# Kernel tuning notes

Hardware: AMD Instinct MI355X
Metric: run time of the kernel (lower is better)

Reference implementation:

```python
import jax, jax.numpy as jnp
import numpy as np

N_EMBD = 768
N_HEAD = 12


def setup_inputs() -> dict:
    key = jax.random.key(0)
    k1, k2, k3, k4, k5 = jax.random.split(key, 5)
    B, T, C = 2, 2048, N_EMBD
    s = 1.0 / np.sqrt(C)
    x = jax.random.normal(k1, (B, T, C), dtype=jnp.float32)
    W_attn = jax.random.uniform(k2, (C, 3 * C), dtype=jnp.float32, minval=-s, maxval=s)
    b_attn = jax.random.uniform(k3, (3 * C,), dtype=jnp.float32, minval=-s, maxval=s)
    W_proj = jax.random.uniform(k4, (C, C), dtype=jnp.float32, minval=-s, maxval=s)
    b_proj = jax.random.uniform(k5, (C,), dtype=jnp.float32, minval=-s, maxval=s)
    return {"x": x, "W_attn": W_attn, "b_attn": b_attn, "W_proj": W_proj, "b_proj": b_proj}


def reference(x, W_attn, b_attn, W_proj, b_proj):
    B, T, C = x.shape
    H = N_HEAD
    D = C // H
    qkv = x @ W_attn + b_attn                      # [B,T,3C]
    q, k, v = jnp.split(qkv, 3, axis=-1)
    q = q.reshape(B, T, H, D).transpose(0, 2, 1, 3)  # [B,H,T,D]
    k = k.reshape(B, T, H, D).transpose(0, 2, 1, 3)
    v = v.reshape(B, T, H, D).transpose(0, 2, 1, 3)
    scale = 1.0 / jnp.sqrt(jnp.asarray(D, dtype=x.dtype))
    scores = jnp.einsum("bhqd,bhkd->bhqk", q, k) * scale  # [B,H,T,T]
    causal = jnp.tril(jnp.ones((T, T), dtype=bool))
    scores = jnp.where(causal, scores, jnp.finfo(x.dtype).min)
    attn = jax.nn.softmax(scores, axis=-1)
    y = jnp.einsum("bhqk,bhkd->bhqd", attn, v)     # [B,H,T,D]
    y = y.transpose(0, 2, 1, 3).reshape(B, T, C)
    return y @ W_proj + b_proj
```

## Files before the change

### kernel.cpp

```cpp
#include <hip/hip_runtime.h>
#include <math.h>

#define N_EMBD 768
#define N_HEAD 12
#define HEAD_DIM 64
#define SEQ 2048
#define BATCH 2

typedef __attribute__((ext_vector_type(8))) short v8s;
typedef __attribute__((ext_vector_type(4))) float v4f;

__device__ __forceinline__ unsigned short f2bf(float f) {
    union { float f; unsigned int u; } x; x.f = f;
    unsigned int u = x.u + 0x7fffu + ((x.u >> 16) & 1u);
    return (unsigned short)(u >> 16);
}
__device__ __forceinline__ float bf2f(unsigned short s) {
    union { unsigned int u; float f; } x; x.u = ((unsigned int)s) << 16;
    return x.f;
}
__device__ __forceinline__ unsigned int pack_bf16(float lo, float hi) {
    unsigned int ul = __float_as_uint(lo) + 0x8000u;
    unsigned int uh = __float_as_uint(hi) + 0x8000u;
    return __builtin_amdgcn_perm(uh, ul, 0x07060302);
}

__device__ __forceinline__ void gload_lds16(const unsigned short* g, unsigned short* l) {
    __builtin_amdgcn_global_load_lds(
        (const __attribute__((address_space(1))) void*)g,
        (__attribute__((address_space(3))) void*)l, 16, 0, 0);
}

#define QSCALE 0.1803368801111396f

__global__ __launch_bounds__(256) void cast_x_kernel(
    const float* __restrict__ in, unsigned short* __restrict__ out)
{
    const int i = (blockIdx.x * 256 + threadIdx.x) * 8;
    const float4 a = *(const float4*)(in + i);
    const float4 b = *(const float4*)(in + i + 4);
    ushort4 s0, s1;
    s0.x = f2bf(a.x); s0.y = f2bf(a.y); s0.z = f2bf(a.z); s0.w = f2bf(a.w);
    s1.x = f2bf(b.x); s1.y = f2bf(b.y); s1.z = f2bf(b.z); s1.w = f2bf(b.w);
    *(ushort4*)(out + i) = s0;
    *(ushort4*)(out + i + 4) = s1;
}

__global__ __launch_bounds__(256) void transpose_cast_kernel(
    const float* __restrict__ in, unsigned short* __restrict__ out, int R, int C)
{
    __shared__ float t[32][33];
    const int bx = blockIdx.x * 32;
    const int by = blockIdx.y * 32;
    const int tx = threadIdx.x & 31, ty = threadIdx.x >> 5;
#pragma unroll
    for (int i = 0; i < 32; i += 8)
        t[ty + i][tx] = in[(size_t)(by + ty + i) * C + bx + tx];
    __syncthreads();
#pragma unroll
    for (int i = 0; i < 32; i += 8)
        out[(size_t)(bx + ty + i) * R + by + tx] = f2bf(t[tx][ty + i]);
}

__global__ __launch_bounds__(256) void qkv_gemm_mfma(
    const unsigned short* __restrict__ A,
    const unsigned short* __restrict__ Bt,
    const float* __restrict__ bias,
    unsigned short* __restrict__ qg,
    unsigned short* __restrict__ kg,
    unsigned short* __restrict__ vg)
{
    __shared__ unsigned short as[128 * 32];
    __shared__ unsigned short bs[128 * 32];
    const int K = 768;
    const int tid = threadIdx.x;
    const int lane = tid & 63;
    const int w = tid >> 6;
    const int wm = w >> 1, wn = w & 1;
    const int quad = lane >> 4, c = lane & 15;
    const int bm = blockIdx.y * 128;
    const int bn = blockIdx.x * 128;

    v4f acc[4][4];
#pragma unroll
    for (int i = 0; i < 4; i++)
#pragma unroll
        for (int j = 0; j < 4; j++) acc[i][j] = (v4f){0.f, 0.f, 0.f, 0.f};

    for (int k0 = 0; k0 < K; k0 += 32) {
        __syncthreads();
#pragma unroll
        for (int p = 0; p < 2; p++) {
            const int idx = p * 256 + tid;
            const int row = idx >> 2;
            const int off = (idx & 3) * 8;
            gload_lds16(A  + (size_t)(bm + row) * K + k0 + off, &as[idx * 8]);
            gload_lds16(Bt + (size_t)(bn + row) * K + k0 + off, &bs[idx * 8]);
        }
        __syncthreads();

        v8s af[4], bf[4];
#pragma unroll
        for (int fm = 0; fm < 4; fm++)
            af[fm] = *(const v8s*)&as[(wm * 64 + fm * 16 + c) * 32 + quad * 8];
#pragma unroll
        for (int fn = 0; fn < 4; fn++)
            bf[fn] = *(const v8s*)&bs[(wn * 64 + fn * 16 + c) * 32 + quad * 8];
#pragma unroll
        for (int fm = 0; fm < 4; fm++)
#pragma unroll
            for (int fn = 0; fn < 4; fn++)
                acc[fm][fn] = __builtin_amdgcn_mfma_f32_16x16x32_bf16(af[fm], bf[fn], acc[fm][fn], 0, 0, 0);
    }

    const int which = bn / N_EMBD;
    const int rem_base = bn - which * N_EMBD;
#pragma unroll
    for (int fm = 0; fm < 4; fm++) {
        const int m0 = bm + wm * 64 + fm * 16 + quad * 4;
        const int b = m0 >> 11;
        const int t0 = m0 & (SEQ - 1);
#pragma unroll
        for (int fn = 0; fn < 4; fn++) {
            const int rem = rem_base + wn * 64 + fn * 16 + c;
            const int h = rem >> 6, d = rem & 63;
            const float bv = bias[bn + wn * 64 + fn * 16 + c];
            const size_t bh = (size_t)(b * N_HEAD + h);
            if (which == 2) {
                ushort4 o;
                o.x = f2bf(acc[fm][fn][0] + bv);
                o.y = f2bf(acc[fm][fn][1] + bv);
                o.z = f2bf(acc[fm][fn][2] + bv);
                o.w = f2bf(acc[fm][fn][3] + bv);
                *(ushort4*)(vg + (bh * 64 + d) * SEQ + t0) = o;
            } else {
                unsigned short* dst = (which == 0) ? qg : kg;
                const float sc = (which == 0) ? QSCALE : 1.0f;
#pragma unroll
                for (int r = 0; r < 4; r++)
                    dst[(bh * SEQ + t0 + r) * 64 + d] = f2bf((acc[fm][fn][r] + bv) * sc);
            }
        }
    }
}

__global__ __launch_bounds__(256) void attn_kernel(
    const unsigned short* __restrict__ qg,
    const unsigned short* __restrict__ kg,
    const unsigned short* __restrict__ vg,
    unsigned short* __restrict__ pO,
    float* __restrict__ pl)
{
    __shared__ __align__(16) unsigned short ks[64 * 64];
    __shared__ __align__(16) unsigned short vs[64 * 64];
    __shared__ __align__(16) unsigned short ps[4][16 * 64];

    const int tid  = threadIdx.x;
    const int w    = tid >> 6;
    const int lane = tid & 63;
    const int quad = lane >> 4;
    const int c    = lane & 15;

    const int bid = (int)blockIdx.x;
    const int bh  = bid % 24;
    const int c2  = 79 - (bid / 24);
    int qt, kc;
    if (c2 < 8)       { qt = c2;                    kc = 0; }
    else if (c2 < 24) { qt = 8 + ((c2 - 8) >> 1);   kc = (c2 - 8) & 1; }
    else if (c2 < 48) { qt = 16 + (c2 - 24) / 3;    kc = (c2 - 24) % 3; }
    else              { qt = 24 + ((c2 - 48) >> 2); kc = (c2 - 48) & 3; }
    const int qbase = qt * 64;

    const unsigned short* qrow = qg + (size_t)bh * SEQ * 64;
    const unsigned short* krow = kg + (size_t)bh * SEQ * 64;
    const unsigned short* vrow = vg + (size_t)bh * 64 * SEQ;

    const unsigned short* qp = qrow + (size_t)(qbase + w * 16 + c) * 64 + quad * 8;
    const v8s bq0 = *(const v8s*)(qp);
    const v8s bq1 = *(const v8s*)(qp + 32);

    const int r0 = tid >> 3;
    const int ch0 = (tid & 7) ^ (r0 & 7);
    const unsigned short* kp0 = krow + (size_t)r0 * 64 + ch0 * 8;
    const unsigned short* vp0 = vrow + (size_t)r0 * SEQ + ch0 * 8;

    const int swz0 = ((quad ^ (c & 7)) * 8);
    const int swz1 = swz0 ^ 32;

    v4f oacc[4];
#pragma unroll
    for (int d = 0; d < 4; d++) oacc[d] = (v4f){0.f, 0.f, 0.f, 0.f};
    float l_acc = 0.f;

    const int q_lane = qbase + w * 16 + c;
    unsigned int* pw32 = (unsigned int*)&ps[w][0];
    const int psq = c & 7;

    const int kt0 = kc * 8;
    const int kt1 = min(kt0 + 8, qt + 1);
    for (int kt = kt0; kt < kt1; kt++) {
        const int key0 = kt * 64;
        __syncthreads();
        gload_lds16(kp0 + (size_t)key0 * 64, &ks[tid * 8]);
        gload_lds16(kp0 + (size_t)(key0 + 32) * 64, &ks[(256 + tid) * 8]);
        gload_lds16(vp0 + key0, &vs[tid * 8]);
        gload_lds16(vp0 + 32 * SEQ + key0, &vs[(256 + tid) * 8]);
        __syncthreads();

        v4f sacc[4];
#pragma unroll
        for (int n = 0; n < 4; n++) {
            const int rb = (n * 16 + c) * 64;
            const v8s ak0 = *(const v8s*)&ks[rb + swz0];
            const v8s ak1 = *(const v8s*)&ks[rb + swz1];
            v4f s = (v4f){0.f, 0.f, 0.f, 0.f};
            s = __builtin_amdgcn_mfma_f32_16x16x32_bf16(ak0, bq0, s, 0, 0, 0);
            s = __builtin_amdgcn_mfma_f32_16x16x32_bf16(ak1, bq1, s, 0, 0, 0);
            sacc[n] = s;
        }

        if (kt == qt) {
            const int kb = key0 + quad * 4;
#pragma unroll
            for (int n = 0; n < 4; n++)
#pragma unroll
                for (int r = 0; r < 4; r++)
                    if (kb + n * 16 + r > q_lane) sacc[n][r] = -1e30f;
        }

#pragma unroll
        for (int n = 0; n < 4; n++) {
            const float p0 = exp2f(sacc[n][0]);
            const float p1 = exp2f(sacc[n][1]);
            const float p2 = exp2f(sacc[n][2]);
            const float p3 = exp2f(sacc[n][3]);
            l_acc += (p0 + p1) + (p2 + p3);
            const int sswz = (2 * n + (quad >> 1)) ^ psq;
            const int dw = c * 32 + sswz * 4 + (quad & 1) * 2;
            pw32[dw]     = pack_bf16(p0, p1);
            pw32[dw + 1] = pack_bf16(p2, p3);
        }

        const v8s ap0 = *(const v8s*)&ps[w][c * 64 + swz0];
        const v8s ap1 = *(const v8s*)&ps[w][c * 64 + swz1];
#pragma unroll
        for (int d = 0; d < 4; d++) {
            const int rb = (d * 16 + c) * 64;
            const v8s bv0 = *(const v8s*)&vs[rb + swz0];
            const v8s bv1 = *(const v8s*)&vs[rb + swz1];
            oacc[d] = __builtin_amdgcn_mfma_f32_16x16x32_bf16(ap0, bv0, oacc[d], 0, 0, 0);
            oacc[d] = __builtin_amdgcn_mfma_f32_16x16x32_bf16(ap1, bv1, oacc[d], 0, 0, 0);
        }
    }

    l_acc += __shfl_xor(l_acc, 16, 64);
    l_acc += __shfl_xor(l_acc, 32, 64);

    const size_t pidx = (size_t)bh * 80 + c2;
    unsigned short* po = pO + pidx * 4096;
#pragma unroll
    for (int r = 0; r < 4; r++) {
        const int row = w * 16 + quad * 4 + r;
#pragma unroll
        for (int d = 0; d < 4; d++)
            po[row * 64 + d * 16 + c] = f2bf(oacc[d][r]);
    }
    if (lane < 16)
        pl[pidx * 64 + w * 16 + c] = l_acc;
}

__global__ __launch_bounds__(256) void combine_kernel(
    const unsigned short* __restrict__ pO,
    const float* __restrict__ pl,
    unsigned short* __restrict__ y)
{
    const int qt = (int)blockIdx.x;
    const int bh = (int)blockIdx.y;
    int base, nc;
    if (qt < 8)       { base = qt;                 nc = 1; }
    else if (qt < 16) { base = 8 + 2 * (qt - 8);   nc = 2; }
    else if (qt < 24) { base = 24 + 3 * (qt - 16); nc = 3; }
    else              { base = 48 + 4 * (qt - 24); nc = 4; }

    const int row = threadIdx.x >> 2;
    const int colg = (threadIdx.x & 3) * 16;

    float denom = 0.f;
    for (int i = 0; i < nc; i++)
        denom += pl[((size_t)bh * 80 + base + i) * 64 + row];
    const float inv = 1.0f / denom;

    float acc[16];
#pragma unroll
    for (int j = 0; j < 16; j++) acc[j] = 0.f;
    for (int i = 0; i < nc; i++) {
        const unsigned short* po = pO + ((size_t)bh * 80 + base + i) * 4096 + row * 64 + colg;
        ushort4 u0 = *(const ushort4*)(po + 0);
        ushort4 u1 = *(const ushort4*)(po + 4);
        ushort4 u2 = *(const ushort4*)(po + 8);
        ushort4 u3 = *(const ushort4*)(po + 12);
        acc[0]  += bf2f(u0.x); acc[1]  += bf2f(u0.y);
        acc[2]  += bf2f(u0.z); acc[3]  += bf2f(u0.w);
        acc[4]  += bf2f(u1.x); acc[5]  += bf2f(u1.y);
        acc[6]  += bf2f(u1.z); acc[7]  += bf2f(u1.w);
        acc[8]  += bf2f(u2.x); acc[9]  += bf2f(u2.y);
        acc[10] += bf2f(u2.z); acc[11] += bf2f(u2.w);
        acc[12] += bf2f(u3.x); acc[13] += bf2f(u3.y);
        acc[14] += bf2f(u3.z); acc[15] += bf2f(u3.w);
    }

    const int b = bh / N_HEAD;
    const int h = bh - b * N_HEAD;
    const int t = qt * 64 + row;
    unsigned short* yr = y + ((size_t)(b * SEQ + t)) * N_EMBD + h * 64 + colg;
    ushort4 o0, o1, o2, o3;
    o0.x = f2bf(acc[0] * inv);  o0.y = f2bf(acc[1] * inv);
    o0.z = f2bf(acc[2] * inv);  o0.w = f2bf(acc[3] * inv);
    o1.x = f2bf(acc[4] * inv);  o1.y = f2bf(acc[5] * inv);
    o1.z = f2bf(acc[6] * inv);  o1.w = f2bf(acc[7] * inv);
    o2.x = f2bf(acc[8] * inv);  o2.y = f2bf(acc[9] * inv);
    o2.z = f2bf(acc[10] * inv); o2.w = f2bf(acc[11] * inv);
    o3.x = f2bf(acc[12] * inv); o3.y = f2bf(acc[13] * inv);
    o3.z = f2bf(acc[14] * inv); o3.w = f2bf(acc[15] * inv);
    *(ushort4*)(yr + 0)  = o0;
    *(ushort4*)(yr + 4)  = o1;
    *(ushort4*)(yr + 8)  = o2;
    *(ushort4*)(yr + 12) = o3;
}

__global__ __launch_bounds__(256) void proj_gemm_mfma(
    const unsigned short* __restrict__ A,
    const unsigned short* __restrict__ Bt,
    const float* __restrict__ bias,
    float* __restrict__ out)
{
    __shared__ unsigned short as[128 * 32];
    __shared__ unsigned short bs[128 * 32];
    const int K = 768;
    const int tid = threadIdx.x;
    const int lane = tid & 63;
    const int w = tid >> 6;
    const int wm = w >> 1, wn = w & 1;
    const int quad = lane >> 4, c = lane & 15;
    const int bm = blockIdx.y * 128;
    const int bn = blockIdx.x * 128;

    v4f acc[4][4];
#pragma unroll
    for (int i = 0; i < 4; i++)
#pragma unroll
        for (int j = 0; j < 4; j++) acc[i][j] = (v4f){0.f, 0.f, 0.f, 0.f};

    for (int k0 = 0; k0 < K; k0 += 32) {
        __syncthreads();
#pragma unroll
        for (int p = 0; p < 2; p++) {
            const int idx = p * 256 + tid;
            const int row = idx >> 2;
            const int off = (idx & 3) * 8;
            gload_lds16(A  + (size_t)(bm + row) * K + k0 + off, &as[idx * 8]);
            gload_lds16(Bt + (size_t)(bn + row) * K + k0 + off, &bs[idx * 8]);
        }
        __syncthreads();

        v8s af[4], bf[4];
#pragma unroll
        for (int fm = 0; fm < 4; fm++)
            af[fm] = *(const v8s*)&as[(wm * 64 + fm * 16 + c) * 32 + quad * 8];
#pragma unroll
        for (int fn = 0; fn < 4; fn++)
            bf[fn] = *(const v8s*)&bs[(wn * 64 + fn * 16 + c) * 32 + quad * 8];
#pragma unroll
        for (int fm = 0; fm < 4; fm++)
#pragma unroll
            for (int fn = 0; fn < 4; fn++)
                acc[fm][fn] = __builtin_amdgcn_mfma_f32_16x16x32_bf16(af[fm], bf[fn], acc[fm][fn], 0, 0, 0);
    }

#pragma unroll
    for (int fm = 0; fm < 4; fm++) {
        const int m0 = bm + wm * 64 + fm * 16 + quad * 4;
#pragma unroll
        for (int fn = 0; fn < 4; fn++) {
            const int n = bn + wn * 64 + fn * 16 + c;
            const float bv = bias[n];
#pragma unroll
            for (int r = 0; r < 4; r++)
                out[(size_t)(m0 + r) * N_EMBD + n] = acc[fm][fn][r] + bv;
        }
    }
}

extern "C" void kernel_launch(void* const* d_in, const int* in_sizes, int n_in,
                              void* d_out, int out_size, void* d_ws, size_t ws_size,
                              hipStream_t stream) {
    const float* x      = (const float*)d_in[0];
    const float* W_attn = (const float*)d_in[1];
    const float* b_attn = (const float*)d_in[2];
    const float* W_proj = (const float*)d_in[3];
    const float* b_proj = (const float*)d_in[4];
    float* out = (float*)d_out;

    const size_t QSZ = (size_t)BATCH * N_HEAD * SEQ * HEAD_DIM;

    unsigned short* base = (unsigned short*)d_ws;
    unsigned short* xb  = base;
    unsigned short* wta = base + QSZ;
    unsigned short* pO  = base;
    float* pl = (float*)(base + (size_t)1920 * 4096);
    unsigned short* wtp = (unsigned short*)(pl + 1920 * 64);
    unsigned short* qg  = wtp + (size_t)N_EMBD * N_EMBD;
    unsigned short* kg  = qg + QSZ;
    unsigned short* vg  = kg + QSZ;
    unsigned short* yb  = vg + QSZ;

    cast_x_kernel<<<dim3((int)(QSZ / (256 * 8))), 256, 0, stream>>>(x, xb);
    transpose_cast_kernel<<<dim3(72, 24), 256, 0, stream>>>(W_attn, wta, N_EMBD, 3 * N_EMBD);
    transpose_cast_kernel<<<dim3(24, 24), 256, 0, stream>>>(W_proj, wtp, N_EMBD, N_EMBD);

    qkv_gemm_mfma<<<dim3(18, 32), 256, 0, stream>>>(xb, wta, b_attn, qg, kg, vg);
    attn_kernel<<<dim3(80 * 24), 256, 0, stream>>>(qg, kg, vg, pO, pl);
    combine_kernel<<<dim3(32, BATCH * N_HEAD), 256, 0, stream>>>(pO, pl, yb);
    proj_gemm_mfma<<<dim3(6, 32), 256, 0, stream>>>(yb, wtp, b_proj, out);
}
```

Measured before the change: 176.5 us.

## Double-buffer LDS tiles in GEMMs and attention, merge prep kernels

The QKV and projection GEMMs and the attention kernel now keep two LDS buffers. Each loop iteration issues the next tile's global-to-LDS loads right after the barrier, so the copy overlaps with the MFMA work on the current tile, and one barrier per iteration is removed. Separately, the x cast and the two weight transpose-cast kernels are merged into one prep kernel launch that picks its task by block index, which saves two launches. The cost is double the LDS per block, which can lower occupancy. Correctness also relies on the barrier waiting for the outstanding async LDS loads.

```diff
diff --git a/kernel.cpp b/kernel.cpp
--- a/kernel.cpp
+++ b/kernel.cpp
@@ -33,25 +33,37 @@
 
 #define QSCALE 0.1803368801111396f
 
-__global__ __launch_bounds__(256) void cast_x_kernel(
-    const float* __restrict__ in, unsigned short* __restrict__ out)
-{
-    const int i = (blockIdx.x * 256 + threadIdx.x) * 8;
-    const float4 a = *(const float4*)(in + i);
-    const float4 b = *(const float4*)(in + i + 4);
-    ushort4 s0, s1;
-    s0.x = f2bf(a.x); s0.y = f2bf(a.y); s0.z = f2bf(a.z); s0.w = f2bf(a.w);
-    s1.x = f2bf(b.x); s1.y = f2bf(b.y); s1.z = f2bf(b.z); s1.w = f2bf(b.w);
-    *(ushort4*)(out + i) = s0;
-    *(ushort4*)(out + i + 4) = s1;
-}
-
-__global__ __launch_bounds__(256) void transpose_cast_kernel(
-    const float* __restrict__ in, unsigned short* __restrict__ out, int R, int C)
+__global__ __launch_bounds__(256) void prep_kernel(
+    const float* __restrict__ x,
+    const float* __restrict__ W_attn,
+    const float* __restrict__ W_proj,
+    unsigned short* __restrict__ xb,
+    unsigned short* __restrict__ wta,
+    unsigned short* __restrict__ wtp)
 {
     __shared__ float t[32][33];
-    const int bx = blockIdx.x * 32;
-    const int by = blockIdx.y * 32;
+    const int blk = (int)blockIdx.x;
+    if (blk < 1536) {
+        const int i = (blk * 256 + threadIdx.x) * 8;
+        const float4 a = *(const float4*)(x + i);
+        const float4 b = *(const float4*)(x + i + 4);
+        ushort4 s0, s1;
+        s0.x = f2bf(a.x); s0.y = f2bf(a.y); s0.z = f2bf(a.z); s0.w = f2bf(a.w);
+        s1.x = f2bf(b.x); s1.y = f2bf(b.y); s1.z = f2bf(b.z); s1.w = f2bf(b.w);
+        *(ushort4*)(xb + i) = s0;
+        *(ushort4*)(xb + i + 4) = s1;
+        return;
+    }
+    const float* in; unsigned short* out; int R, C, bx, by;
+    if (blk < 1536 + 1728) {
+        const int b2 = blk - 1536;
+        in = W_attn; out = wta; R = 768; C = 2304;
+        bx = (b2 % 72) * 32; by = (b2 / 72) * 32;
+    } else {
+        const int b2 = blk - 3264;
+        in = W_proj; out = wtp; R = 768; C = 768;
+        bx = (b2 % 24) * 32; by = (b2 / 24) * 32;
+    }
     const int tx = threadIdx.x & 31, ty = threadIdx.x >> 5;
 #pragma unroll
     for (int i = 0; i < 32; i += 8)
@@ -70,8 +82,8 @@
     unsigned short* __restrict__ kg,
     unsigned short* __restrict__ vg)
 {
-    __shared__ unsigned short as[128 * 32];
-    __shared__ unsigned short bs[128 * 32];
+    __shared__ unsigned short as[2][128 * 32];
+    __shared__ unsigned short bs[2][128 * 32];
     const int K = 768;
     const int tid = threadIdx.x;
     const int lane = tid & 63;
@@ -81,31 +93,42 @@
     const int bm = blockIdx.y * 128;
     const int bn = blockIdx.x * 128;
 
+    const int srow = tid >> 2;
+    const int soff = (tid & 3) * 8;
+    const unsigned short* ap = A  + (size_t)(bm + srow) * K + soff;
+    const unsigned short* bp = Bt + (size_t)(bn + srow) * K + soff;
+    const unsigned short* ap2 = A  + (size_t)(bm + 64 + srow) * K + soff;
+    const unsigned short* bp2 = Bt + (size_t)(bn + 64 + srow) * K + soff;
+
     v4f acc[4][4];
 #pragma unroll
     for (int i = 0; i < 4; i++)
 #pragma unroll
         for (int j = 0; j < 4; j++) acc[i][j] = (v4f){0.f, 0.f, 0.f, 0.f};
 
-    for (int k0 = 0; k0 < K; k0 += 32) {
+    gload_lds16(ap, &as[0][tid * 8]);
+    gload_lds16(ap2, &as[0][(256 + tid) * 8]);
+    gload_lds16(bp, &bs[0][tid * 8]);
+    gload_lds16(bp2, &bs[0][(256 + tid) * 8]);
+
+    int bufi = 0;
+    for (int k0 = 0; k0 < K; k0 += 32, bufi ^= 1) {
         __syncthreads();
-#pragma unroll
-        for (int p = 0; p < 2; p++) {
-            const int idx = p * 256 + tid;
-            const int row = idx >> 2;
-            const int off = (idx & 3) * 8;
-            gload_lds16(A  + (size_t)(bm + row) * K + k0 + off, &as[idx * 8]);
-            gload_lds16(Bt + (size_t)(bn + row) * K + k0 + off, &bs[idx * 8]);
-        }
-        __syncthreads();
+        if (k0 + 32 < K) {
+            const int kn = k0 + 32;
+            gload_lds16(ap + kn, &as[bufi ^ 1][tid * 8]);
+            gload_lds16(ap2 + kn, &as[bufi ^ 1][(256 + tid) * 8]);
+            gload_lds16(bp + kn, &bs[bufi ^ 1][tid * 8]);
+            gload_lds16(bp2 + kn, &bs[bufi ^ 1][(256 + tid) * 8]);
+        }
 
         v8s af[4], bf[4];
 #pragma unroll
         for (int fm = 0; fm < 4; fm++)
-            af[fm] = *(const v8s*)&as[(wm * 64 + fm * 16 + c) * 32 + quad * 8];
+            af[fm] = *(const v8s*)&as[bufi][(wm * 64 + fm * 16 + c) * 32 + quad * 8];
 #pragma unroll
         for (int fn = 0; fn < 4; fn++)
-            bf[fn] = *(const v8s*)&bs[(wn * 64 + fn * 16 + c) * 32 + quad * 8];
+            bf[fn] = *(const v8s*)&bs[bufi][(wn * 64 + fn * 16 + c) * 32 + quad * 8];
 #pragma unroll
         for (int fm = 0; fm < 4; fm++)
 #pragma unroll
@@ -151,8 +174,8 @@
     unsigned short* __restrict__ pO,
     float* __restrict__ pl)
 {
-    __shared__ __align__(16) unsigned short ks[64 * 64];
-    __shared__ __align__(16) unsigned short vs[64 * 64];
+    __shared__ __align__(16) unsigned short ks[2][64 * 64];
+    __shared__ __align__(16) unsigned short vs[2][64 * 64];
     __shared__ __align__(16) unsigned short ps[4][16 * 64];
 
     const int tid  = threadIdx.x;
@@ -198,21 +221,34 @@
 
     const int kt0 = kc * 8;
     const int kt1 = min(kt0 + 8, qt + 1);
+
+    {
+        const int key0 = kt0 * 64;
+        const int b = kt0 & 1;
+        gload_lds16(kp0 + (size_t)key0 * 64, &ks[b][tid * 8]);
+        gload_lds16(kp0 + (size_t)(key0 + 32) * 64, &ks[b][(256 + tid) * 8]);
+        gload_lds16(vp0 + key0, &vs[b][tid * 8]);
+        gload_lds16(vp0 + 32 * SEQ + key0, &vs[b][(256 + tid) * 8]);
+    }
+
     for (int kt = kt0; kt < kt1; kt++) {
+        const int b = kt & 1;
+        __syncthreads();
+        if (kt + 1 < kt1) {
+            const int key0n = (kt + 1) * 64;
+            gload_lds16(kp0 + (size_t)key0n * 64, &ks[b ^ 1][tid * 8]);
+            gload_lds16(kp0 + (size_t)(key0n + 32) * 64, &ks[b ^ 1][(256 + tid) * 8]);
+            gload_lds16(vp0 + key0n, &vs[b ^ 1][tid * 8]);
+            gload_lds16(vp0 + 32 * SEQ + key0n, &vs[b ^ 1][(256 + tid) * 8]);
+        }
         const int key0 = kt * 64;
-        __syncthreads();
-        gload_lds16(kp0 + (size_t)key0 * 64, &ks[tid * 8]);
-        gload_lds16(kp0 + (size_t)(key0 + 32) * 64, &ks[(256 + tid) * 8]);
-        gload_lds16(vp0 + key0, &vs[tid * 8]);
-        gload_lds16(vp0 + 32 * SEQ + key0, &vs[(256 + tid) * 8]);
-        __syncthreads();
 
         v4f sacc[4];
 #pragma unroll
         for (int n = 0; n < 4; n++) {
             const int rb = (n * 16 + c) * 64;
-            const v8s ak0 = *(const v8s*)&ks[rb + swz0];
-            const v8s ak1 = *(const v8s*)&ks[rb + swz1];
+            const v8s ak0 = *(const v8s*)&ks[b][rb + swz0];
+            const v8s ak1 = *(const v8s*)&ks[b][rb + swz1];
             v4f s = (v4f){0.f, 0.f, 0.f, 0.f};
             s = __builtin_amdgcn_mfma_f32_16x16x32_bf16(ak0, bq0, s, 0, 0, 0);
             s = __builtin_amdgcn_mfma_f32_16x16x32_bf16(ak1, bq1, s, 0, 0, 0);
@@ -246,8 +282,8 @@
 #pragma unroll
         for (int d = 0; d < 4; d++) {
             const int rb = (d * 16 + c) * 64;
-            const v8s bv0 = *(const v8s*)&vs[rb + swz0];
-            const v8s bv1 = *(const v8s*)&vs[rb + swz1];
+            const v8s bv0 = *(const v8s*)&vs[b][rb + swz0];
+            const v8s bv1 = *(const v8s*)&vs[b][rb + swz1];
             oacc[d] = __builtin_amdgcn_mfma_f32_16x16x32_bf16(ap0, bv0, oacc[d], 0, 0, 0);
             oacc[d] = __builtin_amdgcn_mfma_f32_16x16x32_bf16(ap1, bv1, oacc[d], 0, 0, 0);
         }
@@ -334,8 +370,8 @@
     const float* __restrict__ bias,
     float* __restrict__ out)
 {
-    __shared__ unsigned short as[128 * 32];
-    __shared__ unsigned short bs[128 * 32];
+    __shared__ unsigned short as[2][128 * 32];
+    __shared__ unsigned short bs[2][128 * 32];
     const int K = 768;
     const int tid = threadIdx.x;
     const int lane = tid & 63;
@@ -345,31 +381,42 @@
     const int bm = blockIdx.y * 128;
     const int bn = blockIdx.x * 128;
 
+    const int srow = tid >> 2;
+    const int soff = (tid & 3) * 8;
+    const unsigned short* ap = A  + (size_t)(bm + srow) * K + soff;
+    const unsigned short* bp = Bt + (size_t)(bn + srow) * K + soff;
+    const unsigned short* ap2 = A  + (size_t)(bm + 64 + srow) * K + soff;
+    const unsigned short* bp2 = Bt + (size_t)(bn + 64 + srow) * K + soff;
+
     v4f acc[4][4];
 #pragma unroll
     for (int i = 0; i < 4; i++)
 #pragma unroll
         for (int j = 0; j < 4; j++) acc[i][j] = (v4f){0.f, 0.f, 0.f, 0.f};
 
-    for (int k0 = 0; k0 < K; k0 += 32) {
+    gload_lds16(ap, &as[0][tid * 8]);
+    gload_lds16(ap2, &as[0][(256 + tid) * 8]);
+    gload_lds16(bp, &bs[0][tid * 8]);
+    gload_lds16(bp2, &bs[0][(256 + tid) * 8]);
+
+    int bufi = 0;
+    for (int k0 = 0; k0 < K; k0 += 32, bufi ^= 1) {
         __syncthreads();
-#pragma unroll
-        for (int p = 0; p < 2; p++) {
-            const int idx = p * 256 + tid;
-            const int row = idx >> 2;
-            const int off = (idx & 3) * 8;
-            gload_lds16(A  + (size_t)(bm + row) * K + k0 + off, &as[idx * 8]);
-            gload_lds16(Bt + (size_t)(bn + row) * K + k0 + off, &bs[idx * 8]);
-        }
-        __syncthreads();
+        if (k0 + 32 < K) {
+            const int kn = k0 + 32;
+            gload_lds16(ap + kn, &as[bufi ^ 1][tid * 8]);
+            gload_lds16(ap2 + kn, &as[bufi ^ 1][(256 + tid) * 8]);
+            gload_lds16(bp + kn, &bs[bufi ^ 1][tid * 8]);
+            gload_lds16(bp2 + kn, &bs[bufi ^ 1][(256 + tid) * 8]);
+        }
 
         v8s af[4], bf[4];
 #pragma unroll
         for (int fm = 0; fm < 4; fm++)
-            af[fm] = *(const v8s*)&as[(wm * 64 + fm * 16 + c) * 32 + quad * 8];
+            af[fm] = *(const v8s*)&as[bufi][(wm * 64 + fm * 16 + c) * 32 + quad * 8];
 #pragma unroll
         for (int fn = 0; fn < 4; fn++)
-            bf[fn] = *(const v8s*)&bs[(wn * 64 + fn * 16 + c) * 32 + quad * 8];
+            bf[fn] = *(const v8s*)&bs[bufi][(wn * 64 + fn * 16 + c) * 32 + quad * 8];
 #pragma unroll
         for (int fm = 0; fm < 4; fm++)
 #pragma unroll
@@ -414,10 +461,7 @@
     unsigned short* vg  = kg + QSZ;
     unsigned short* yb  = vg + QSZ;
 
-    cast_x_kernel<<<dim3((int)(QSZ / (256 * 8))), 256, 0, stream>>>(x, xb);
-    transpose_cast_kernel<<<dim3(72, 24), 256, 0, stream>>>(W_attn, wta, N_EMBD, 3 * N_EMBD);
-    transpose_cast_kernel<<<dim3(24, 24), 256, 0, stream>>>(W_proj, wtp, N_EMBD, N_EMBD);
-
+    prep_kernel<<<dim3(3840), 256, 0, stream>>>(x, W_attn, W_proj, xb, wta, wtp);
     qkv_gemm_mfma<<<dim3(18, 32), 256, 0, stream>>>(xb, wta, b_attn, qg, kg, vg);
     attn_kernel<<<dim3(80 * 24), 256, 0, stream>>>(qg, kg, vg, pO, pl);
     combine_kernel<<<dim3(32, BATCH * N_HEAD), 256, 0, stream>>>(pO, pl, yb);
```

After: 162.1 us. 8.2% less time.
